# Kernel tuning notes

Hardware: AMD Instinct MI355X
Metric: run time of the kernel (lower is better)

The kernel has to match this reference:

```python
import jax, jax.numpy as jnp
import numpy as np

NUM_USERS = 100000
NUM_POIS = 50000
N = NUM_USERS + NUM_POIS   # total graph nodes (users then pois)
D = 128                    # embedding_dim
POI_D = 320                # poi_embed_dim
E = 2000000                # number of edges
B = 1024                   # batch of user ids
NEG_SLOPE = 0.2


def setup_inputs() -> dict:
    key = jax.random.key(0)
    ks = jax.random.split(key, 12)
    stdv = 1.0 / np.sqrt(D)  # module resets all params to U(-stdv, stdv)
    u = lambda k, s: jax.random.uniform(k, s, jnp.float32, -stdv, stdv)
    return {
        "user_idx": jax.random.randint(ks[0], (B,), 0, NUM_USERS),
        "poi_embeddings": jax.random.normal(ks[1], (NUM_POIS, POI_D), jnp.float32),
        "edge_index": jax.random.randint(ks[2], (2, E), 0, N),
        "user_table": u(ks[3], (NUM_USERS, D)),
        "Wp": u(ks[4], (POI_D, D)), "bp": u(ks[5], (D,)),
        "W1": u(ks[6], (D, D)), "b1": u(ks[7], (D,)),
        "W2": u(ks[8], (D, D)), "b2": u(ks[9], (D,)),
        "Wf": u(ks[10], (D, D)), "bf": u(ks[11], (D,)),
    }


def _leaky(x):
    return jnp.where(x >= 0, x, NEG_SLOPE * x)


def _gcn_conv(x, W, b, src, dst, dinv):
    # PyG GCNConv: h = xW; out_i = sum_{j->i} dinv_j*dinv_i*h_j + dinv_i^2*h_i + b
    h = x @ W
    norm = dinv[src] * dinv[dst]                       # [E]
    agg = jax.ops.segment_sum(h[src] * norm[:, None], dst, num_segments=N)
    agg = agg + (dinv * dinv)[:, None] * h             # self-loop term
    return agg + b


def reference(user_idx, poi_embeddings, edge_index, user_table,
              Wp, bp, W1, b1, W2, b2, Wf, bf):
    src, dst = edge_index[0], edge_index[1]
    # degree with self-loops (edge weight 1)
    deg = 1.0 + jax.ops.segment_sum(jnp.ones((E,), jnp.float32), dst, num_segments=N)
    dinv = jax.lax.rsqrt(deg)

    poi_feats = poi_embeddings @ Wp + bp               # [NUM_POIS, D]
    x = jnp.concatenate([user_table, poi_feats], axis=0)  # [N, D]
    x = _leaky(_gcn_conv(x, W1, b1, src, dst, dinv))
    # dropout p=0.2 is identity in eval mode
    x = _leaky(_gcn_conv(x, W2, b2, src, dst, dinv))

    out = x[user_idx] + user_table[user_idx]           # [B, D]
    return out @ Wf + bf
```

## Files before the change

### kernel.cpp

```cpp
#include <hip/hip_runtime.h>

#define NUSERS 100000
#define NPOIS  50000
#define NN     150000
#define DD     128
#define EE     2000000
#define BB     1024
#define NT2M   32768

#define CH_IPT 16
#define CH_BLK 256
#define CHUNK  (CH_IPT * CH_BLK)

#define HR   3
#define HS   50000
#define HSI  12500
#define HC   85
#define HPER 23532

typedef __attribute__((ext_vector_type(8))) short short8;
typedef __attribute__((ext_vector_type(4))) float f32x4;
typedef unsigned short ushort_t;

__device__ __forceinline__ ushort_t f2bf(float x) {
    union { float f; unsigned u; } a; a.f = x;
    unsigned r = a.u + 0x7fffu + ((a.u >> 16) & 1u);
    return (ushort_t)(r >> 16);
}
__device__ __forceinline__ float bf2f(ushort_t h) {
    union { unsigned u; float f; } a; a.u = ((unsigned)h) << 16;
    return a.f;
}

__global__ void k_mark(const int* __restrict__ uidx, int* __restrict__ mask_s2,
                       int* __restrict__ mask_t2) {
    int b = blockIdx.x * blockDim.x + threadIdx.x;
    if (b < BB) { int u = uidx[b]; mask_s2[u] = 1; mask_t2[u] = 1; }
}

__global__ __launch_bounds__(1024)
void k_hist3(const int* __restrict__ src, const int* __restrict__ dst,
             const int* __restrict__ mask_s2, int* __restrict__ mask_t2,
             int* __restrict__ slab) {
    __shared__ int h[HSI];
    const int r = blockIdx.x / HC, c = blockIdx.x % HC;
    const int lo = r * HS;
    const int tid = threadIdx.x;
    for (int i = tid; i < HSI; i += 1024) h[i] = 0;
    __syncthreads();
    const int e0 = c * HPER;
    const int e1 = min(e0 + HPER, EE);
    for (int e = e0 + tid * 4; e < e1; e += 4096) {
        int4 d4 = *(const int4*)&dst[e];
        unsigned u0 = (unsigned)(d4.x - lo), u1 = (unsigned)(d4.y - lo);
        unsigned u2 = (unsigned)(d4.z - lo), u3 = (unsigned)(d4.w - lo);
        if (u0 < (unsigned)HS) atomicAdd(&h[u0 >> 2], 1 << ((u0 & 3) << 3));
        if (u1 < (unsigned)HS) atomicAdd(&h[u1 >> 2], 1 << ((u1 & 3) << 3));
        if (u2 < (unsigned)HS) atomicAdd(&h[u2 >> 2], 1 << ((u2 & 3) << 3));
        if (u3 < (unsigned)HS) atomicAdd(&h[u3 >> 2], 1 << ((u3 & 3) << 3));
    }
    const int m0 = e0 + r * (HPER / 3);
    const int m1 = min(e0 + (r + 1) * (HPER / 3), EE);
    for (int e = m0 + tid * 4; e < m1; e += 4096) {
        int4 d4 = *(const int4*)&dst[e];
        int q0 = mask_s2[d4.x], q1 = mask_s2[d4.y];
        int q2 = mask_s2[d4.z], q3 = mask_s2[d4.w];
        if (q0 | q1 | q2 | q3) {
            int4 s4 = *(const int4*)&src[e];
            if (q0) mask_t2[s4.x] = 1;
            if (q1) mask_t2[s4.y] = 1;
            if (q2) mask_t2[s4.z] = 1;
            if (q3) mask_t2[s4.w] = 1;
        }
    }
    __syncthreads();
    int* out = slab + (size_t)blockIdx.x * HSI;
    for (int i = tid; i < HSI; i += 1024) out[i] = h[i];
}

__global__ void k_reduce3(const int* __restrict__ slab, int* __restrict__ cnt,
                          float* __restrict__ dinv) {
    int i = blockIdx.x * blockDim.x + threadIdx.x;
    if (i >= HR * HSI) return;
    int r = i / HSI, ii = i - r * HSI;
    const int* p = slab + (size_t)(r * HC) * HSI + ii;
    int s = 0;
    #pragma unroll
    for (int c = 0; c < HC; ++c) s += p[(size_t)c * HSI];
    int n0 = r * HS + (ii << 2);
    int4 cv;
    cv.x = s & 255; cv.y = (s >> 8) & 255; cv.z = (s >> 16) & 255; cv.w = (s >> 24) & 255;
    *(int4*)&cnt[n0] = cv;
    float4 dv;
    dv.x = rsqrtf(1.0f + (float)cv.x); dv.y = rsqrtf(1.0f + (float)cv.y);
    dv.z = rsqrtf(1.0f + (float)cv.z); dv.w = rsqrtf(1.0f + (float)cv.w);
    *(float4*)&dinv[n0] = dv;
}

__global__ __launch_bounds__(256)
void k_slots(const int* __restrict__ mask_s2, const int* __restrict__ mask_t2,
             int* __restrict__ slot_s2, int* __restrict__ slot_t2,
             int* __restrict__ rev_s2, int* __restrict__ rev_t2,
             int* __restrict__ ctr) {
    __shared__ int s_wcnt_t[4], s_wcnt_s[4];
    __shared__ int s_base_t, s_base_s;
    const int tid = threadIdx.x;
    const int lane = tid & 63;
    const int wid = tid >> 6;
    const int nch = (NN + CHUNK - 1) / CHUNK;
    for (int c = blockIdx.x; c < nch; c += gridDim.x) {
        const int n0 = c * CHUNK;
        unsigned hbits_t = 0, hbits_s = 0;
        int wt = 0, ws = 0;
        #pragma unroll
        for (int i = 0; i < CH_IPT; ++i) {
            int n = n0 + i * CH_BLK + tid;
            bool inb = (n < NN);
            bool ht = inb && (mask_t2[n] != 0);
            bool hs = inb && (mask_s2[n] != 0);
            unsigned long long mt = __ballot(ht);
            unsigned long long ms = __ballot(hs);
            if (ht) hbits_t |= (1u << i);
            if (hs) hbits_s |= (1u << i);
            wt += __popcll(mt); ws += __popcll(ms);
        }
        if (lane == 0) { s_wcnt_t[wid] = wt; s_wcnt_s[wid] = ws; }
        __syncthreads();
        if (tid == 0) s_base_t = atomicAdd(&ctr[0], s_wcnt_t[0]+s_wcnt_t[1]+s_wcnt_t[2]+s_wcnt_t[3]);
        if (tid == 1) s_base_s = atomicAdd(&ctr[1], s_wcnt_s[0]+s_wcnt_s[1]+s_wcnt_s[2]+s_wcnt_s[3]);
        __syncthreads();
        int off_t = s_base_t, off_s = s_base_s;
        for (int w = 0; w < wid; ++w) { off_t += s_wcnt_t[w]; off_s += s_wcnt_s[w]; }
        #pragma unroll
        for (int i = 0; i < CH_IPT; ++i) {
            unsigned long long mt = __ballot((hbits_t >> i) & 1);
            unsigned long long ms = __ballot((hbits_s >> i) & 1);
            int n = n0 + i * CH_BLK + tid;
            if ((hbits_t >> i) & 1) {
                int p = off_t + __popcll(mt & ((1ull << lane) - 1ull));
                slot_t2[n] = p; rev_t2[p] = n;
            }
            if ((hbits_s >> i) & 1) {
                int p = off_s + __popcll(ms & ((1ull << lane) - 1ull));
                slot_s2[n] = p; rev_s2[p] = n;
            }
            off_t += __popcll(mt); off_s += __popcll(ms);
        }
        __syncthreads();
    }
}

__global__ __launch_bounds__(1024)
void k_scan2(const int* __restrict__ ctr, const int* __restrict__ rev_t2,
             const int* __restrict__ rev_s2, const int* __restrict__ cnt,
             int* __restrict__ ptr1, int* __restrict__ cur1, int* __restrict__ cur1b,
             int* __restrict__ ptr2, int* __restrict__ cur2, int* __restrict__ cur2b) {
    __shared__ int wsum[16];
    __shared__ int s_carry;
    const int which = blockIdx.x;
    const int n = ctr[which];
    const int* rev = which ? rev_s2 : rev_t2;
    int* ptr = which ? ptr2 : ptr1;
    int* cur = which ? cur2 : cur1;
    int* curB = which ? cur2b : cur1b;
    const int tid = threadIdx.x;
    const int lane = tid & 63, wid = tid >> 6;
    if (tid == 0) s_carry = 0;
    __syncthreads();
    for (int base = 0; base < n; base += 4096) {
        int i0 = base + tid * 4;
        int v[4];
        #pragma unroll
        for (int k = 0; k < 4; ++k) {
            int i = i0 + k;
            v[k] = (i < n) ? cnt[rev[i]] : 0;
        }
        int tsum = v[0] + v[1] + v[2] + v[3];
        int x = tsum;
        #pragma unroll
        for (int s = 1; s < 64; s <<= 1) {
            int y = __shfl_up(x, s, 64);
            if (lane >= s) x += y;
        }
        if (lane == 63) wsum[wid] = x;
        __syncthreads();
        if (wid == 0) {
            int wv = (lane < 16) ? wsum[lane] : 0;
            #pragma unroll
            for (int s = 1; s < 16; s <<= 1) {
                int y = __shfl_up(wv, s, 64);
                if (lane >= s) wv += y;
            }
            if (lane < 16) wsum[lane] = wv;
        }
        __syncthreads();
        int carry = s_carry;
        int woff = (wid > 0) ? wsum[wid - 1] : 0;
        int excl = carry + woff + (x - tsum);
        #pragma unroll
        for (int k = 0; k < 4; ++k) {
            int i = i0 + k;
            if (i < n) { ptr[i] = excl; cur[i] = excl; curB[i] = excl + v[k]; }
            excl += v[k];
        }
        __syncthreads();
        if (tid == 0) s_carry = carry + wsum[15];
        __syncthreads();
    }
}

__global__ void k_scatter(const int* __restrict__ src, const int* __restrict__ dst,
                          const int* __restrict__ slot_s2, const int* __restrict__ slot_t2,
                          int* __restrict__ cur1, int* __restrict__ cur1b,
                          int* __restrict__ cur2,
                          int* __restrict__ csr1, int* __restrict__ csr2) {
    int stride = gridDim.x * blockDim.x;
    for (int e = blockIdx.x * blockDim.x + threadIdx.x; e < EE; e += stride) {
        int d = dst[e];
        int sl1 = slot_t2[d];
        int sl2 = slot_s2[d];
        if ((sl1 | sl2) != -1 || sl1 >= 0 || sl2 >= 0) {
            if (sl1 >= 0 || sl2 >= 0) {
                int s = src[e];
                if (sl1 >= 0) {
                    if (s < NUSERS) { int p = atomicAdd(&cur1[sl1], 1);   csr1[p] = s; }
                    else            { int p = atomicAdd(&cur1b[sl1], -1); csr1[p - 1] = s; }
                }
                if (sl2 >= 0) { int p = atomicAdd(&cur2[sl2], 1); csr2[p] = s; }
            }
        }
    }
}

__global__ void k_wpw1(const float* __restrict__ Wp, const float* __restrict__ W1,
                       float* __restrict__ WpW1) {
    int i = blockIdx.x * blockDim.x + threadIdx.x;
    if (i >= 320 * 128) return;
    int r = i >> 7, c = i & 127;
    float s = 0.f;
    for (int k = 0; k < 128; ++k) s = fmaf(Wp[r * 128 + k], W1[k * 128 + c], s);
    WpW1[i] = s;
}

__global__ void k_bpw1(const float* __restrict__ bp, const float* __restrict__ W1,
                       float* __restrict__ bpW1) {
    int c = threadIdx.x;
    float s = 0.f;
    for (int k = 0; k < 128; ++k) s = fmaf(bp[k], W1[k * 128 + c], s);
    bpW1[c] = s;
}

__global__ void k_wprepW(const float* __restrict__ W1, const float* __restrict__ WpW1,
                         const float* __restrict__ bpW1,
                         ushort_t* __restrict__ Th, ushort_t* __restrict__ Tl) {
    int i = blockIdx.x * blockDim.x + threadIdx.x;
    if (i >= 128 * 512) return;
    int n = i >> 9, k = i & 511;
    float x = (k < 128) ? W1[k * 128 + n]
            : (k < 448) ? WpW1[(k - 128) * 128 + n]
            : (k == 448) ? bpW1[n] : 0.f;
    ushort_t h = f2bf(x);
    ushort_t l = f2bf(x - bf2f(h));
    Th[n * 512 + k] = h; Tl[n * 512 + k] = l;
}

__global__ void k_wprep2(const float* __restrict__ W2, const float* __restrict__ Wf,
                         ushort_t* __restrict__ T2h, ushort_t* __restrict__ T2l,
                         ushort_t* __restrict__ Tfh, ushort_t* __restrict__ Tfl) {
    int i = blockIdx.x * blockDim.x + threadIdx.x;
    if (i >= 2 * 128 * 128) return;
    int wsel = i >> 14, j = i & 16383;
    const float* W = wsel ? Wf : W2;
    ushort_t* Th = wsel ? Tfh : T2h;
    ushort_t* Tl = wsel ? Tfl : T2l;
    int k = j >> 7, n = j & 127;
    float x = W[j];
    ushort_t h = f2bf(x);
    ushort_t l = f2bf(x - bf2f(h));
    Th[n * 128 + k] = h; Tl[n * 128 + k] = l;
}

__global__ __launch_bounds__(256)
void k_agg1(const int* __restrict__ ctr, const int* __restrict__ rev_t2,
            const int* __restrict__ ptr1, const int* __restrict__ cur1,
            const int* __restrict__ cnt, const int* __restrict__ csr1,
            const float* __restrict__ dinv,
            const float* __restrict__ ut, const float* __restrict__ poi,
            ushort_t* __restrict__ Ah, ushort_t* __restrict__ Al) {
    const int nt2 = min(ctr[0], NT2M);
    const int lane = threadIdx.x & 63;
    const int w0id = (blockIdx.x * blockDim.x + threadIdx.x) >> 6;
    const int nw = (gridDim.x * blockDim.x) >> 6;
    for (int slot = w0id; slot < nt2; slot += nw) {
        int node = rev_t2[slot];
        float dn = dinv[node], dd = dn * dn;
        float u0 = 0.f, u1 = 0.f, p0 = 0.f, p1 = 0.f, p2 = 0.f, p3 = 0.f, p4 = 0.f, sP = 0.f;
        if (node < NUSERS) {
            const float2 v = *(const float2*)&ut[((size_t)node << 7) + (lane << 1)];
            u0 = dd * v.x; u1 = dd * v.y;
        } else {
            const float* pr = poi + (size_t)(node - NUSERS) * 320;
            p0 = dd * pr[lane]; p1 = dd * pr[lane + 64]; p2 = dd * pr[lane + 128];
            p3 = dd * pr[lane + 192]; p4 = dd * pr[lane + 256];
            sP = dd;
        }
        const int j0 = ptr1[slot];
        const int sp = cur1[slot];
        const int jend = j0 + cnt[node];
        for (int j = j0; j < sp; j += 4) {
            int i1 = min(j + 1, sp - 1), i2 = min(j + 2, sp - 1), i3 = min(j + 3, sp - 1);
            int s0 = csr1[j], s1 = csr1[i1], s2 = csr1[i2], s3 = csr1[i3];
            float w0 = dn * dinv[s0];
            float w1 = (j + 1 < sp) ? dn * dinv[s1] : 0.f;
            float w2 = (j + 2 < sp) ? dn * dinv[s2] : 0.f;
            float w3 = (j + 3 < sp) ? dn * dinv[s3] : 0.f;
            const float2 v0 = *(const float2*)&ut[((size_t)s0 << 7) + (lane << 1)];
            const float2 v1 = *(const float2*)&ut[((size_t)s1 << 7) + (lane << 1)];
            const float2 v2 = *(const float2*)&ut[((size_t)s2 << 7) + (lane << 1)];
            const float2 v3 = *(const float2*)&ut[((size_t)s3 << 7) + (lane << 1)];
            u0 = fmaf(w0, v0.x, u0); u1 = fmaf(w0, v0.y, u1);
            u0 = fmaf(w1, v1.x, u0); u1 = fmaf(w1, v1.y, u1);
            u0 = fmaf(w2, v2.x, u0); u1 = fmaf(w2, v2.y, u1);
            u0 = fmaf(w3, v3.x, u0); u1 = fmaf(w3, v3.y, u1);
        }
        for (int j = sp; j < jend; j += 3) {
            int i1 = min(j + 1, jend - 1), i2 = min(j + 2, jend - 1);
            int s0 = csr1[j], s1 = csr1[i1], s2 = csr1[i2];
            float w0 = dn * dinv[s0];
            float w1 = (j + 1 < jend) ? dn * dinv[s1] : 0.f;
            float w2 = (j + 2 < jend) ? dn * dinv[s2] : 0.f;
            const float* pa = poi + (size_t)(s0 - NUSERS) * 320;
            const float* pb = poi + (size_t)(s1 - NUSERS) * 320;
            const float* pc = poi + (size_t)(s2 - NUSERS) * 320;
            p0 = fmaf(w0, pa[lane], p0);       p1 = fmaf(w0, pa[lane + 64], p1);
            p2 = fmaf(w0, pa[lane + 128], p2); p3 = fmaf(w0, pa[lane + 192], p3);
            p4 = fmaf(w0, pa[lane + 256], p4);
            p0 = fmaf(w1, pb[lane], p0);       p1 = fmaf(w1, pb[lane + 64], p1);
            p2 = fmaf(w1, pb[lane + 128], p2); p3 = fmaf(w1, pb[lane + 192], p3);
            p4 = fmaf(w1, pb[lane + 256], p4);
            p0 = fmaf(w2, pc[lane], p0);       p1 = fmaf(w2, pc[lane + 64], p1);
            p2 = fmaf(w2, pc[lane + 128], p2); p3 = fmaf(w2, pc[lane + 192], p3);
            p4 = fmaf(w2, pc[lane + 256], p4);
            sP += w0 + w1 + w2;
        }
        size_t base = (size_t)slot << 9;
        ushort_t h, l;
        h = f2bf(u0); l = f2bf(u0 - bf2f(h));
        Ah[base + (lane << 1)] = h; Al[base + (lane << 1)] = l;
        h = f2bf(u1); l = f2bf(u1 - bf2f(h));
        Ah[base + (lane << 1) + 1] = h; Al[base + (lane << 1) + 1] = l;
        float pv[5] = {p0, p1, p2, p3, p4};
        #pragma unroll
        for (int q = 0; q < 5; ++q) {
            h = f2bf(pv[q]); l = f2bf(pv[q] - bf2f(h));
            Ah[base + 128 + lane + (q << 6)] = h; Al[base + 128 + lane + (q << 6)] = l;
        }
        float t = (lane == 0) ? sP : 0.f;
        h = f2bf(t); l = f2bf(t - bf2f(h));
        Ah[base + 448 + lane] = h; Al[base + 448 + lane] = l;
    }
}

template<int KSTEPS, bool LEAKY>
__global__ __launch_bounds__(256)
void gemm_bf(const ushort_t* __restrict__ Ah_g, const ushort_t* __restrict__ Al_g,
             const ushort_t* __restrict__ BTh, const ushort_t* __restrict__ BTl,
             const float* __restrict__ bias, float* __restrict__ C,
             int M, const int* __restrict__ Mdyn)
{
    constexpr int K = KSTEPS * 64;
    __shared__ ushort_t Bh[128 * 64], Bl[128 * 64];
    __shared__ ushort_t Ahs[64 * 64], Als[64 * 64];
    const int tid = threadIdx.x;
    const int wave = tid >> 6, lane = tid & 63;
    const int wr = wave >> 1, wc = wave & 1;
    const int lr = lane & 15, g = lane >> 4;
    if (Mdyn) M = min(*Mdyn, NT2M);
    const int ntiles = (M + 63) >> 6;
    for (int tile = blockIdx.x; tile < ntiles; tile += gridDim.x) {
        const int row0 = tile << 6;
        f32x4 acc[2][4];
        #pragma unroll
        for (int a = 0; a < 2; ++a)
            #pragma unroll
            for (int b = 0; b < 4; ++b) acc[a][b] = (f32x4){0.f, 0.f, 0.f, 0.f};
        for (int kc = 0; kc < K; kc += 64) {
            __syncthreads();
            #pragma unroll
            for (int i = 0; i < 4; ++i) {
                int c = tid + i * 256;
                int n = c >> 3, kq = c & 7;
                size_t go = (size_t)n * K + kc + kq * 8;
                int boff = n * 128 + ((kq * 16) ^ ((n & 7) << 4));
                *(int4*)((char*)Bh + boff) = *(const int4*)&BTh[go];
                *(int4*)((char*)Bl + boff) = *(const int4*)&BTl[go];
            }
            #pragma unroll
            for (int i = 0; i < 2; ++i) {
                int c = tid + i * 256;
                int r = c >> 3, kq = c & 7;
                int row = row0 + r;
                int4 va = {0, 0, 0, 0}, vb = {0, 0, 0, 0};
                if (row < M) {
                    size_t go = (size_t)row * K + kc + kq * 8;
                    va = *(const int4*)&Ah_g[go];
                    vb = *(const int4*)&Al_g[go];
                }
                int aoff = r * 128 + ((kq * 16) ^ ((r & 7) << 4));
                *(int4*)((char*)Ahs + aoff) = va;
                *(int4*)((char*)Als + aoff) = vb;
            }
            __syncthreads();
            #pragma unroll
            for (int kk2 = 0; kk2 < 2; ++kk2) {
                short8 afh[2], afl[2];
                #pragma unroll
                for (int rt = 0; rt < 2; ++rt) {
                    int ar = wr * 32 + rt * 16 + lr;
                    int off = ar * 128 + ((kk2 * 64 + g * 16) ^ ((ar & 7) << 4));
                    afh[rt] = *(short8*)((char*)Ahs + off);
                    afl[rt] = *(short8*)((char*)Als + off);
                }
                #pragma unroll
                for (int ct = 0; ct < 4; ++ct) {
                    int bn = wc * 64 + ct * 16 + lr;
                    int off = bn * 128 + ((kk2 * 64 + g * 16) ^ ((bn & 7) << 4));
                    short8 bfh = *(short8*)((char*)Bh + off);
                    short8 bfl = *(short8*)((char*)Bl + off);
                    #pragma unroll
                    for (int rt = 0; rt < 2; ++rt) {
                        acc[rt][ct] = __builtin_amdgcn_mfma_f32_16x16x32_bf16(afh[rt], bfh, acc[rt][ct], 0, 0, 0);
                        acc[rt][ct] = __builtin_amdgcn_mfma_f32_16x16x32_bf16(afh[rt], bfl, acc[rt][ct], 0, 0, 0);
                        acc[rt][ct] = __builtin_amdgcn_mfma_f32_16x16x32_bf16(afl[rt], bfh, acc[rt][ct], 0, 0, 0);
                    }
                }
            }
        }
        #pragma unroll
        for (int ct = 0; ct < 4; ++ct) {
            int col = wc * 64 + ct * 16 + lr;
            float bv = bias[col];
            #pragma unroll
            for (int rt = 0; rt < 2; ++rt) {
                #pragma unroll
                for (int v = 0; v < 4; ++v) {
                    int row = row0 + wr * 32 + rt * 16 + g * 4 + v;
                    if (row < M) {
                        float o = acc[rt][ct][v] + bv;
                        if (LEAKY) o = o >= 0.f ? o : 0.2f * o;
                        C[(size_t)row * 128 + col] = o;
                    }
                }
            }
        }
    }
}

__global__ __launch_bounds__(256)
void k_agg2(const int* __restrict__ ctr, const int* __restrict__ rev_s2,
            const int* __restrict__ ptr2, const int* __restrict__ cnt,
            const int* __restrict__ csr2, const int* __restrict__ slot_t2,
            const float* __restrict__ dinv, const float* __restrict__ x1c,
            ushort_t* __restrict__ X2h, ushort_t* __restrict__ X2l) {
    const int ns2 = ctr[1];
    const int lane = threadIdx.x & 63;
    const int col = lane << 1;
    const int w0id = (blockIdx.x * blockDim.x + threadIdx.x) >> 6;
    const int nw = (gridDim.x * blockDim.x) >> 6;
    for (int slot = w0id; slot < ns2; slot += nw) {
        int node = rev_s2[slot];
        float dn = dinv[node], dd = dn * dn;
        float2 acc = *(const float2*)&x1c[((size_t)slot_t2[node] << 7) + col];
        acc.x *= dd; acc.y *= dd;
        const int j0 = ptr2[slot];
        const int jend = j0 + cnt[node];
        for (int j = j0; j < jend; j += 4) {
            int i1 = min(j + 1, jend - 1), i2 = min(j + 2, jend - 1), i3 = min(j + 3, jend - 1);
            int s0 = csr2[j], s1 = csr2[i1], s2 = csr2[i2], s3 = csr2[i3];
            float w0 = dn * dinv[s0];
            float w1 = (j + 1 < jend) ? dn * dinv[s1] : 0.f;
            float w2 = (j + 2 < jend) ? dn * dinv[s2] : 0.f;
            float w3 = (j + 3 < jend) ? dn * dinv[s3] : 0.f;
            const float2 h0 = *(const float2*)&x1c[((size_t)slot_t2[s0] << 7) + col];
            const float2 h1 = *(const float2*)&x1c[((size_t)slot_t2[s1] << 7) + col];
            const float2 h2 = *(const float2*)&x1c[((size_t)slot_t2[s2] << 7) + col];
            const float2 h3 = *(const float2*)&x1c[((size_t)slot_t2[s3] << 7) + col];
            acc.x = fmaf(w0, h0.x, acc.x); acc.y = fmaf(w0, h0.y, acc.y);
            acc.x = fmaf(w1, h1.x, acc.x); acc.y = fmaf(w1, h1.y, acc.y);
            acc.x = fmaf(w2, h2.x, acc.x); acc.y = fmaf(w2, h2.y, acc.y);
            acc.x = fmaf(w3, h3.x, acc.x); acc.y = fmaf(w3, h3.y, acc.y);
        }
        size_t base = ((size_t)slot << 7) + col;
        ushort_t h0 = f2bf(acc.x), l0 = f2bf(acc.x - bf2f(h0));
        ushort_t h1 = f2bf(acc.y), l1 = f2bf(acc.y - bf2f(h1));
        X2h[base] = h0; X2h[base + 1] = h1;
        X2l[base] = l0; X2l[base + 1] = l1;
    }
}

__global__ void k_finalA(const int* __restrict__ uidx, const int* __restrict__ slot_s2,
                         const float* __restrict__ x2c, const float* __restrict__ ut,
                         ushort_t* __restrict__ Fh, ushort_t* __restrict__ Fl) {
    int i = blockIdx.x * blockDim.x + threadIdx.x;
    if (i >= BB * 64) return;
    int b = i >> 6, l = i & 63;
    int u = uidx[b];
    const float2 xv = *(const float2*)&x2c[((size_t)slot_s2[u] << 7) + (l << 1)];
    const float2 uv = *(const float2*)&ut[((size_t)u << 7) + (l << 1)];
    float a0 = xv.x + uv.x, a1 = xv.y + uv.y;
    size_t base = ((size_t)b << 7) + (l << 1);
    ushort_t h0 = f2bf(a0), l0 = f2bf(a0 - bf2f(h0));
    ushort_t h1 = f2bf(a1), l1 = f2bf(a1 - bf2f(h1));
    Fh[base] = h0; Fh[base + 1] = h1;
    Fl[base] = l0; Fl[base + 1] = l1;
}

extern "C" void kernel_launch(void* const* d_in, const int* in_sizes, int n_in,
                              void* d_out, int out_size, void* d_ws, size_t ws_size,
                              hipStream_t stream) {
    const int*   uidx    = (const int*)d_in[0];
    const float* poi     = (const float*)d_in[1];
    const int*   src     = (const int*)d_in[2];
    const int*   dst     = ((const int*)d_in[2]) + EE;
    const float* usert   = (const float*)d_in[3];
    const float* Wp      = (const float*)d_in[4];
    const float* bp      = (const float*)d_in[5];
    const float* W1      = (const float*)d_in[6];
    const float* b1      = (const float*)d_in[7];
    const float* W2      = (const float*)d_in[8];
    const float* b2      = (const float*)d_in[9];
    const float* Wf      = (const float*)d_in[10];
    const float* bf      = (const float*)d_in[11];
    float* out = (float*)d_out;

    char* w = (char*)d_ws;
    size_t off = 0;
    auto alloc = [&](size_t bytes) -> void* {
        void* p = w + off;
        off = (off + bytes + 255) & ~(size_t)255;
        return p;
    };
    float* dinv    = (float*)alloc((size_t)NN * 4);
    int*   cnt     = (int*)  alloc((size_t)NN * 4);
    int*   mask_s2 = (int*)  alloc((size_t)NN * 4);
    int*   mask_t2 = (int*)  alloc((size_t)NN * 4);
    int*   slot_s2 = (int*)  alloc((size_t)NN * 4);
    int*   slot_t2 = (int*)  alloc((size_t)NN * 4);
    int*   rev_t2  = (int*)  alloc((size_t)NN * 4);
    int*   rev_s2  = (int*)  alloc((size_t)BB * 4);
    int*   ptr1    = (int*)  alloc((size_t)(NN + 1) * 4);
    int*   cur1    = (int*)  alloc((size_t)(NN + 1) * 4);
    int*   cur1b   = (int*)  alloc((size_t)(NN + 1) * 4);
    int*   ptr2    = (int*)  alloc((size_t)(BB + 2) * 4);
    int*   cur2    = (int*)  alloc((size_t)(BB + 2) * 4);
    int*   cur2b   = (int*)  alloc((size_t)(BB + 2) * 4);
    int*   ctr     = (int*)  alloc(256);
    int*   csr1    = (int*)  alloc((size_t)EE * 4);
    int*   csr2    = (int*)  alloc((size_t)EE * 4);
    int*   slab    = (int*)  alloc((size_t)HR * HC * HSI * 4);
    float* WpW1    = (float*)alloc((size_t)320 * 128 * 4);
    float* bpW1    = (float*)alloc((size_t)128 * 4);
    ushort_t* WTh  = (ushort_t*)alloc((size_t)128 * 512 * 2);
    ushort_t* WTl  = (ushort_t*)alloc((size_t)128 * 512 * 2);
    ushort_t* W2Th = (ushort_t*)alloc((size_t)128 * 128 * 2);
    ushort_t* W2Tl = (ushort_t*)alloc((size_t)128 * 128 * 2);
    ushort_t* WfTh = (ushort_t*)alloc((size_t)128 * 128 * 2);
    ushort_t* WfTl = (ushort_t*)alloc((size_t)128 * 128 * 2);
    ushort_t* Ah   = (ushort_t*)alloc((size_t)NT2M * 512 * 2);
    ushort_t* Al   = (ushort_t*)alloc((size_t)NT2M * 512 * 2);
    float* x1c     = (float*)alloc((size_t)NT2M * 128 * 4);
    ushort_t* X2h  = (ushort_t*)alloc((size_t)2048 * 128 * 2);
    ushort_t* X2l  = (ushort_t*)alloc((size_t)2048 * 128 * 2);
    float* x2c     = (float*)alloc((size_t)2048 * 128 * 4);
    ushort_t* Fh   = (ushort_t*)alloc((size_t)BB * 128 * 2);
    ushort_t* Fl   = (ushort_t*)alloc((size_t)BB * 128 * 2);
    if (off > ws_size) return;

    hipMemsetAsync(mask_s2, 0, (size_t)NN * 4, stream);
    hipMemsetAsync(mask_t2, 0, (size_t)NN * 4, stream);
    hipMemsetAsync(slot_s2, 0xFF, (size_t)NN * 4, stream);
    hipMemsetAsync(slot_t2, 0xFF, (size_t)NN * 4, stream);
    hipMemsetAsync(ctr, 0, 256, stream);

    k_wpw1  <<<160, 256, 0, stream>>>(Wp, W1, WpW1);
    k_bpw1  <<<1, 128, 0, stream>>>(bp, W1, bpW1);
    k_wprepW<<<256, 256, 0, stream>>>(W1, WpW1, bpW1, WTh, WTl);
    k_wprep2<<<128, 256, 0, stream>>>(W2, Wf, W2Th, W2Tl, WfTh, WfTl);

    k_mark   <<<(BB + 255) / 256, 256, 0, stream>>>(uidx, mask_s2, mask_t2);
    k_hist3  <<<HR * HC, 1024, 0, stream>>>(src, dst, mask_s2, mask_t2, slab);
    k_reduce3<<<(HR * HSI + 255) / 256, 256, 0, stream>>>(slab, cnt, dinv);

    k_slots<<<(NN + CHUNK - 1) / CHUNK, 256, 0, stream>>>(mask_s2, mask_t2, slot_s2, slot_t2,
                                                          rev_s2, rev_t2, ctr);
    k_scan2<<<2, 1024, 0, stream>>>(ctr, rev_t2, rev_s2, cnt,
                                    ptr1, cur1, cur1b, ptr2, cur2, cur2b);
    k_scatter<<<2048, 256, 0, stream>>>(src, dst, slot_s2, slot_t2,
                                        cur1, cur1b, cur2, csr1, csr2);

    k_agg1<<<2048, 256, 0, stream>>>(ctr, rev_t2, ptr1, cur1, cnt, csr1, dinv,
                                     usert, poi, Ah, Al);
    gemm_bf<8, true><<<240, 256, 0, stream>>>(Ah, Al, WTh, WTl, b1, x1c, 0, ctr + 0);

    k_agg2<<<256, 256, 0, stream>>>(ctr, rev_s2, ptr2, cnt, csr2, slot_t2, dinv, x1c, X2h, X2l);
    gemm_bf<2, true><<<16, 256, 0, stream>>>(X2h, X2l, W2Th, W2Tl, b2, x2c, 0, ctr + 1);

    k_finalA<<<(BB * 64 + 255) / 256, 256, 0, stream>>>(uidx, slot_s2, x2c, usert, Fh, Fl);
    gemm_bf<2, false><<<16, 256, 0, stream>>>(Fh, Fl, WfTh, WfTl, bf, out, BB, nullptr);
}
```

Measured before the change: 201.7 us.

## Reuse layer-1 CSR for layer-2 aggregation and unroll gather loops

Drops the separate second CSR (csr2/ptr2/cur2) and the second scan block. Layer-2 aggregation now indexes the layer-1 CSR through slot_t2, since every layer-2 target is also a layer-1 target. This halves the scatter's atomic and write traffic and removes one 8 MB buffer. The gather loops in agg1 and agg2 are also restructured into unguarded 8/4-wide bodies with scalar tails, replacing the clamped-index, predicated loads. Because the edges within each layer-1 row are split into user and POI segments, agg2 reads them in a different order, so float summation order changes slightly.

Result: faster. 185.3 us (-8.1%).

```diff
diff --git a/kernel.cpp b/kernel.cpp
--- a/kernel.cpp
+++ b/kernel.cpp
@@ -151,18 +151,12 @@
 }
 
 __global__ __launch_bounds__(1024)
-void k_scan2(const int* __restrict__ ctr, const int* __restrict__ rev_t2,
-             const int* __restrict__ rev_s2, const int* __restrict__ cnt,
-             int* __restrict__ ptr1, int* __restrict__ cur1, int* __restrict__ cur1b,
-             int* __restrict__ ptr2, int* __restrict__ cur2, int* __restrict__ cur2b) {
+void k_scan1(const int* __restrict__ ctr, const int* __restrict__ rev_t2,
+             const int* __restrict__ cnt,
+             int* __restrict__ ptr1, int* __restrict__ cur1, int* __restrict__ cur1b) {
     __shared__ int wsum[16];
     __shared__ int s_carry;
-    const int which = blockIdx.x;
-    const int n = ctr[which];
-    const int* rev = which ? rev_s2 : rev_t2;
-    int* ptr = which ? ptr2 : ptr1;
-    int* cur = which ? cur2 : cur1;
-    int* curB = which ? cur2b : cur1b;
+    const int n = min(ctr[0], NT2M);
     const int tid = threadIdx.x;
     const int lane = tid & 63, wid = tid >> 6;
     if (tid == 0) s_carry = 0;
@@ -173,7 +167,7 @@
         #pragma unroll
         for (int k = 0; k < 4; ++k) {
             int i = i0 + k;
-            v[k] = (i < n) ? cnt[rev[i]] : 0;
+            v[k] = (i < n) ? cnt[rev_t2[i]] : 0;
         }
         int tsum = v[0] + v[1] + v[2] + v[3];
         int x = tsum;
@@ -200,7 +194,7 @@
         #pragma unroll
         for (int k = 0; k < 4; ++k) {
             int i = i0 + k;
-            if (i < n) { ptr[i] = excl; cur[i] = excl; curB[i] = excl + v[k]; }
+            if (i < n) { ptr1[i] = excl; cur1[i] = excl; cur1b[i] = excl + v[k]; }
             excl += v[k];
         }
         __syncthreads();
@@ -210,24 +204,16 @@
 }
 
 __global__ void k_scatter(const int* __restrict__ src, const int* __restrict__ dst,
-                          const int* __restrict__ slot_s2, const int* __restrict__ slot_t2,
+                          const int* __restrict__ slot_t2,
                           int* __restrict__ cur1, int* __restrict__ cur1b,
-                          int* __restrict__ cur2,
-                          int* __restrict__ csr1, int* __restrict__ csr2) {
+                          int* __restrict__ csr1) {
     int stride = gridDim.x * blockDim.x;
     for (int e = blockIdx.x * blockDim.x + threadIdx.x; e < EE; e += stride) {
-        int d = dst[e];
-        int sl1 = slot_t2[d];
-        int sl2 = slot_s2[d];
-        if ((sl1 | sl2) != -1 || sl1 >= 0 || sl2 >= 0) {
-            if (sl1 >= 0 || sl2 >= 0) {
-                int s = src[e];
-                if (sl1 >= 0) {
-                    if (s < NUSERS) { int p = atomicAdd(&cur1[sl1], 1);   csr1[p] = s; }
-                    else            { int p = atomicAdd(&cur1b[sl1], -1); csr1[p - 1] = s; }
-                }
-                if (sl2 >= 0) { int p = atomicAdd(&cur2[sl2], 1); csr2[p] = s; }
-            }
+        int sl1 = slot_t2[dst[e]];
+        if (sl1 >= 0) {
+            int s = src[e];
+            if (s < NUSERS) { int p = atomicAdd(&cur1[sl1], 1);   csr1[p] = s; }
+            else            { int p = atomicAdd(&cur1b[sl1], -1); csr1[p - 1] = s; }
         }
     }
 }
@@ -307,13 +293,33 @@
         const int j0 = ptr1[slot];
         const int sp = cur1[slot];
         const int jend = j0 + cnt[node];
-        for (int j = j0; j < sp; j += 4) {
-            int i1 = min(j + 1, sp - 1), i2 = min(j + 2, sp - 1), i3 = min(j + 3, sp - 1);
-            int s0 = csr1[j], s1 = csr1[i1], s2 = csr1[i2], s3 = csr1[i3];
-            float w0 = dn * dinv[s0];
-            float w1 = (j + 1 < sp) ? dn * dinv[s1] : 0.f;
-            float w2 = (j + 2 < sp) ? dn * dinv[s2] : 0.f;
-            float w3 = (j + 3 < sp) ? dn * dinv[s3] : 0.f;
+        int j = j0;
+        for (; j + 8 <= sp; j += 8) {
+            int s0 = csr1[j],     s1 = csr1[j + 1], s2 = csr1[j + 2], s3 = csr1[j + 3];
+            int s4 = csr1[j + 4], s5 = csr1[j + 5], s6 = csr1[j + 6], s7 = csr1[j + 7];
+            float w0 = dn * dinv[s0], w1 = dn * dinv[s1], w2 = dn * dinv[s2], w3 = dn * dinv[s3];
+            float w4 = dn * dinv[s4], w5 = dn * dinv[s5], w6 = dn * dinv[s6], w7 = dn * dinv[s7];
+            const float2 v0 = *(const float2*)&ut[((size_t)s0 << 7) + (lane << 1)];
+            const float2 v1 = *(const float2*)&ut[((size_t)s1 << 7) + (lane << 1)];
+            const float2 v2 = *(const float2*)&ut[((size_t)s2 << 7) + (lane << 1)];
+            const float2 v3 = *(const float2*)&ut[((size_t)s3 << 7) + (lane << 1)];
+            const float2 v4 = *(const float2*)&ut[((size_t)s4 << 7) + (lane << 1)];
+            const float2 v5 = *(const float2*)&ut[((size_t)s5 << 7) + (lane << 1)];
+            const float2 v6 = *(const float2*)&ut[((size_t)s6 << 7) + (lane << 1)];
+            const float2 v7 = *(const float2*)&ut[((size_t)s7 << 7) + (lane << 1)];
+            u0 = fmaf(w0, v0.x, u0); u1 = fmaf(w0, v0.y, u1);
+            u0 = fmaf(w1, v1.x, u0); u1 = fmaf(w1, v1.y, u1);
+            u0 = fmaf(w2, v2.x, u0); u1 = fmaf(w2, v2.y, u1);
+            u0 = fmaf(w3, v3.x, u0); u1 = fmaf(w3, v3.y, u1);
+            u0 = fmaf(w4, v4.x, u0); u1 = fmaf(w4, v4.y, u1);
+            u0 = fmaf(w5, v5.x, u0); u1 = fmaf(w5, v5.y, u1);
+            u0 = fmaf(w6, v6.x, u0); u1 = fmaf(w6, v6.y, u1);
+            u0 = fmaf(w7, v7.x, u0); u1 = fmaf(w7, v7.y, u1);
+        }
+        for (; j + 4 <= sp; j += 4) {
+            int s0 = csr1[j], s1 = csr1[j + 1], s2 = csr1[j + 2], s3 = csr1[j + 3];
+            float w0 = dn * dinv[s0], w1 = dn * dinv[s1];
+            float w2 = dn * dinv[s2], w3 = dn * dinv[s3];
             const float2 v0 = *(const float2*)&ut[((size_t)s0 << 7) + (lane << 1)];
             const float2 v1 = *(const float2*)&ut[((size_t)s1 << 7) + (lane << 1)];
             const float2 v2 = *(const float2*)&ut[((size_t)s2 << 7) + (lane << 1)];
@@ -323,12 +329,15 @@
             u0 = fmaf(w2, v2.x, u0); u1 = fmaf(w2, v2.y, u1);
             u0 = fmaf(w3, v3.x, u0); u1 = fmaf(w3, v3.y, u1);
         }
-        for (int j = sp; j < jend; j += 3) {
-            int i1 = min(j + 1, jend - 1), i2 = min(j + 2, jend - 1);
-            int s0 = csr1[j], s1 = csr1[i1], s2 = csr1[i2];
-            float w0 = dn * dinv[s0];
-            float w1 = (j + 1 < jend) ? dn * dinv[s1] : 0.f;
-            float w2 = (j + 2 < jend) ? dn * dinv[s2] : 0.f;
+        for (; j < sp; ++j) {
+            int s = csr1[j];
+            float w = dn * dinv[s];
+            const float2 v = *(const float2*)&ut[((size_t)s << 7) + (lane << 1)];
+            u0 = fmaf(w, v.x, u0); u1 = fmaf(w, v.y, u1);
+        }
+        for (j = sp; j + 3 <= jend; j += 3) {
+            int s0 = csr1[j], s1 = csr1[j + 1], s2 = csr1[j + 2];
+            float w0 = dn * dinv[s0], w1 = dn * dinv[s1], w2 = dn * dinv[s2];
             const float* pa = poi + (size_t)(s0 - NUSERS) * 320;
             const float* pb = poi + (size_t)(s1 - NUSERS) * 320;
             const float* pc = poi + (size_t)(s2 - NUSERS) * 320;
@@ -342,6 +351,15 @@
             p2 = fmaf(w2, pc[lane + 128], p2); p3 = fmaf(w2, pc[lane + 192], p3);
             p4 = fmaf(w2, pc[lane + 256], p4);
             sP += w0 + w1 + w2;
+        }
+        for (; j < jend; ++j) {
+            int s = csr1[j];
+            float w = dn * dinv[s];
+            const float* pr = poi + (size_t)(s - NUSERS) * 320;
+            p0 = fmaf(w, pr[lane], p0);       p1 = fmaf(w, pr[lane + 64], p1);
+            p2 = fmaf(w, pr[lane + 128], p2); p3 = fmaf(w, pr[lane + 192], p3);
+            p4 = fmaf(w, pr[lane + 256], p4);
+            sP += w;
         }
         size_t base = (size_t)slot << 9;
         ushort_t h, l;
@@ -458,8 +476,8 @@
 
 __global__ __launch_bounds__(256)
 void k_agg2(const int* __restrict__ ctr, const int* __restrict__ rev_s2,
-            const int* __restrict__ ptr2, const int* __restrict__ cnt,
-            const int* __restrict__ csr2, const int* __restrict__ slot_t2,
+            const int* __restrict__ ptr1, const int* __restrict__ cnt,
+            const int* __restrict__ csr1, const int* __restrict__ slot_t2,
             const float* __restrict__ dinv, const float* __restrict__ x1c,
             ushort_t* __restrict__ X2h, ushort_t* __restrict__ X2l) {
     const int ns2 = ctr[1];
@@ -469,18 +487,17 @@
     const int nw = (gridDim.x * blockDim.x) >> 6;
     for (int slot = w0id; slot < ns2; slot += nw) {
         int node = rev_s2[slot];
+        int tsl = slot_t2[node];
         float dn = dinv[node], dd = dn * dn;
-        float2 acc = *(const float2*)&x1c[((size_t)slot_t2[node] << 7) + col];
+        float2 acc = *(const float2*)&x1c[((size_t)tsl << 7) + col];
         acc.x *= dd; acc.y *= dd;
-        const int j0 = ptr2[slot];
+        const int j0 = ptr1[tsl];
         const int jend = j0 + cnt[node];
-        for (int j = j0; j < jend; j += 4) {
-            int i1 = min(j + 1, jend - 1), i2 = min(j + 2, jend - 1), i3 = min(j + 3, jend - 1);
-            int s0 = csr2[j], s1 = csr2[i1], s2 = csr2[i2], s3 = csr2[i3];
-            float w0 = dn * dinv[s0];
-            float w1 = (j + 1 < jend) ? dn * dinv[s1] : 0.f;
-            float w2 = (j + 2 < jend) ? dn * dinv[s2] : 0.f;
-            float w3 = (j + 3 < jend) ? dn * dinv[s3] : 0.f;
+        int j = j0;
+        for (; j + 4 <= jend; j += 4) {
+            int s0 = csr1[j], s1 = csr1[j + 1], s2 = csr1[j + 2], s3 = csr1[j + 3];
+            float w0 = dn * dinv[s0], w1 = dn * dinv[s1];
+            float w2 = dn * dinv[s2], w3 = dn * dinv[s3];
             const float2 h0 = *(const float2*)&x1c[((size_t)slot_t2[s0] << 7) + col];
             const float2 h1 = *(const float2*)&x1c[((size_t)slot_t2[s1] << 7) + col];
             const float2 h2 = *(const float2*)&x1c[((size_t)slot_t2[s2] << 7) + col];
@@ -489,6 +506,13 @@
             acc.x = fmaf(w1, h1.x, acc.x); acc.y = fmaf(w1, h1.y, acc.y);
             acc.x = fmaf(w2, h2.x, acc.x); acc.y = fmaf(w2, h2.y, acc.y);
             acc.x = fmaf(w3, h3.x, acc.x); acc.y = fmaf(w3, h3.y, acc.y);
+        }
+        for (; j < jend; ++j) {
+            int s = csr1[j];
+            float w = dn * dinv[s];
+            const float2 h = *(const float2*)&x1c[((size_t)slot_t2[s] << 7) + col];
+            acc.x = fmaf(w, h.x, acc.x);
+            acc.y = fmaf(w, h.y, acc.y);
         }
         size_t base = ((size_t)slot << 7) + col;
         ushort_t h0 = f2bf(acc.x), l0 = f2bf(acc.x - bf2f(h0));
@@ -548,15 +572,11 @@
     int*   slot_t2 = (int*)  alloc((size_t)NN * 4);
     int*   rev_t2  = (int*)  alloc((size_t)NN * 4);
     int*   rev_s2  = (int*)  alloc((size_t)BB * 4);
-    int*   ptr1    = (int*)  alloc((size_t)(NN + 1) * 4);
-    int*   cur1    = (int*)  alloc((size_t)(NN + 1) * 4);
-    int*   cur1b   = (int*)  alloc((size_t)(NN + 1) * 4);
-    int*   ptr2    = (int*)  alloc((size_t)(BB + 2) * 4);
-    int*   cur2    = (int*)  alloc((size_t)(BB + 2) * 4);
-    int*   cur2b   = (int*)  alloc((size_t)(BB + 2) * 4);
+    int*   ptr1    = (int*)  alloc((size_t)(NT2M + 1) * 4);
+    int*   cur1    = (int*)  alloc((size_t)(NT2M + 1) * 4);
+    int*   cur1b   = (int*)  alloc((size_t)(NT2M + 1) * 4);
     int*   ctr     = (int*)  alloc(256);
     int*   csr1    = (int*)  alloc((size_t)EE * 4);
-    int*   csr2    = (int*)  alloc((size_t)EE * 4);
     int*   slab    = (int*)  alloc((size_t)HR * HC * HSI * 4);
     float* WpW1    = (float*)alloc((size_t)320 * 128 * 4);
     float* bpW1    = (float*)alloc((size_t)128 * 4);
@@ -593,16 +613,14 @@
 
     k_slots<<<(NN + CHUNK - 1) / CHUNK, 256, 0, stream>>>(mask_s2, mask_t2, slot_s2, slot_t2,
                                                           rev_s2, rev_t2, ctr);
-    k_scan2<<<2, 1024, 0, stream>>>(ctr, rev_t2, rev_s2, cnt,
-                                    ptr1, cur1, cur1b, ptr2, cur2, cur2b);
-    k_scatter<<<2048, 256, 0, stream>>>(src, dst, slot_s2, slot_t2,
-                                        cur1, cur1b, cur2, csr1, csr2);
+    k_scan1<<<1, 1024, 0, stream>>>(ctr, rev_t2, cnt, ptr1, cur1, cur1b);
+    k_scatter<<<2048, 256, 0, stream>>>(src, dst, slot_t2, cur1, cur1b, csr1);
 
     k_agg1<<<2048, 256, 0, stream>>>(ctr, rev_t2, ptr1, cur1, cnt, csr1, dinv,
                                      usert, poi, Ah, Al);
     gemm_bf<8, true><<<240, 256, 0, stream>>>(Ah, Al, WTh, WTl, b1, x1c, 0, ctr + 0);
 
-    k_agg2<<<256, 256, 0, stream>>>(ctr, rev_s2, ptr2, cnt, csr2, slot_t2, dinv, x1c, X2h, X2l);
+    k_agg2<<<256, 256, 0, stream>>>(ctr, rev_s2, ptr1, cnt, csr1, slot_t2, dinv, x1c, X2h, X2l);
     gemm_bf<2, true><<<16, 256, 0, stream>>>(X2h, X2l, W2Th, W2Tl, b2, x2c, 0, ctr + 1);
 
     k_finalA<<<(BB * 64 + 255) / 256, 256, 0, stream>>>(uidx, slot_s2, x2c, usert, Fh, Fl);
```
